# Optimization experiments

Hardware: AMD Instinct MI355X
Metric: run time of the kernel (lower is better)

## Reference

```python
import jax, jax.numpy as jnp
import numpy as np

N = 20000      # nodes
E = 160000     # edges
IN = 128       # in_channels
H = 16         # heads
C = 32         # hidden_channels (per-head dim)
HC = H * C     # 512
ED = 93        # edge_dim
B = 64         # graphs in batch


def setup_inputs() -> dict:
    key = jax.random.key(0)
    ks = jax.random.split(key, 32)
    w = lambda i, shape: jax.random.normal(ks[i], shape, dtype=jnp.float32) * 0.05
    inp = {
        "x": jax.random.normal(ks[0], (N, IN), dtype=jnp.float32),
        "edge_attr": jax.random.normal(ks[1], (E, ED), dtype=jnp.float32),
        "edge_index": jax.random.randint(ks[2], (2, E), 0, N),
        # sorted batch assignment; every graph id 0..B-1 is present
        "batch": (jnp.arange(N) * B) // N,
        # transformer1: in=IN
        "t1_Wq": w(3, (IN, HC)), "t1_bq": jnp.zeros((HC,), jnp.float32),
        "t1_Wk": w(4, (IN, HC)), "t1_bk": jnp.zeros((HC,), jnp.float32),
        "t1_Wv": w(5, (IN, HC)), "t1_bv": jnp.zeros((HC,), jnp.float32),
        "t1_We": w(6, (ED, HC)),
        "t1_Ws": w(7, (IN, HC)), "t1_bs": jnp.zeros((HC,), jnp.float32),
        # transformer2: in=HC
        "t2_Wq": w(8, (HC, HC)), "t2_bq": jnp.zeros((HC,), jnp.float32),
        "t2_Wk": w(9, (HC, HC)), "t2_bk": jnp.zeros((HC,), jnp.float32),
        "t2_Wv": w(10, (HC, HC)), "t2_bv": jnp.zeros((HC,), jnp.float32),
        "t2_We": w(11, (ED, HC)),
        "t2_Ws": w(12, (HC, HC)), "t2_bs": jnp.zeros((HC,), jnp.float32),
        # MLP head: fc1 (hidden*32 -> hidden*8), fc2 (hidden*8 -> hidden)
        "fc1_W": w(13, (2 * HC, 8 * C)), "fc1_b": jnp.zeros((8 * C,), jnp.float32),
        "fc2_W": w(14, (8 * C, C)), "fc2_b": jnp.zeros((C,), jnp.float32),
    }
    return inp


def _tconv(x, src, dst, edge_attr, Wq, bq, Wk, bk, Wv, bv, We, Ws, bs):
    # PyG TransformerConv, concat=True, beta=False, root_weight=True
    n = x.shape[0]
    q = (x @ Wq + bq).reshape(n, H, C)
    k = (x @ Wk + bk).reshape(n, H, C)
    v = (x @ Wv + bv).reshape(n, H, C)
    e = (edge_attr @ We).reshape(-1, H, C)          # lin_edge has no bias
    kj = k[src] + e                                  # [E,H,C]
    alpha = jnp.einsum('ehc,ehc->eh', q[dst], kj) / jnp.sqrt(jnp.float32(C))
    # segment softmax over incoming edges of each destination node
    amax = jax.ops.segment_max(alpha, dst, num_segments=n)
    ex = jnp.exp(alpha - amax[dst])
    denom = jax.ops.segment_sum(ex, dst, num_segments=n)
    a = ex / denom[dst]                              # [E,H]
    msg = (v[src] + e) * a[:, :, None]               # [E,H,C]
    agg = jax.ops.segment_sum(msg.reshape(-1, HC), dst, num_segments=n)
    return agg + x @ Ws + bs                         # root/skip connection


def _pool(x, batch):
    counts = jax.ops.segment_sum(jnp.ones((x.shape[0],), x.dtype), batch, num_segments=B)
    mean = jax.ops.segment_sum(x, batch, num_segments=B) / jnp.maximum(counts, 1.0)[:, None]
    mx = jax.ops.segment_max(x, batch, num_segments=B)
    return jnp.concatenate([mean, mx], axis=1)


def reference(x, edge_attr, edge_index, batch,
              t1_Wq, t1_bq, t1_Wk, t1_bk, t1_Wv, t1_bv, t1_We, t1_Ws, t1_bs,
              t2_Wq, t2_bq, t2_Wk, t2_bk, t2_Wv, t2_bv, t2_We, t2_Ws, t2_bs,
              fc1_W, fc1_b, fc2_W, fc2_b):
    src, dst = edge_index[0], edge_index[1]
    x1 = jax.nn.leaky_relu(_tconv(x, src, dst, edge_attr,
                                  t1_Wq, t1_bq, t1_Wk, t1_bk, t1_Wv, t1_bv,
                                  t1_We, t1_Ws, t1_bs), negative_slope=0.2)
    x3 = _pool(x1, batch)
    x2 = jax.nn.leaky_relu(_tconv(x1, src, dst, edge_attr,
                                  t2_Wq, t2_bq, t2_Wk, t2_bk, t2_Wv, t2_bv,
                                  t2_We, t2_Ws, t2_bs), negative_slope=0.2)
    x4 = _pool(x2, batch)
    h = x3 + x4                                      # [B, 2*HC]
    h = jax.nn.relu(h @ fc1_W + fc1_b)               # dropout = identity (eval)
    out = h @ fc2_W + fc2_b                          # [B, C]
    return out
```

## Files before the change

### kernel.cpp

```cpp
#include <hip/hip_runtime.h>
#include <cstdint>
#include <cstddef>

#define N_NODES 20000
#define N_EDGES 160000
#define IN_CH   128
#define NH      16
#define CD      32
#define HC      512
#define ED      93
#define EDP     96
#define NB      64
#define NCAT    2048
#define NSLICE  8
#define DEGSLK  2048

typedef __attribute__((ext_vector_type(8))) short short8;
typedef __attribute__((ext_vector_type(4))) float f32x4;
typedef unsigned short ushort_t;


__device__ inline ushort_t f2bf(float f) {
    unsigned int u = __float_as_uint(f);
    u = (u + 0x7FFF + ((u >> 16) & 1)) >> 16;
    return (ushort_t)u;
}
__device__ inline float bf2f(ushort_t u) {
    return __uint_as_float((unsigned)u << 16);
}
__device__ inline void unpack8(uint4 u, float* o) {
    o[0] = bf2f((ushort_t)(u.x & 0xffff)); o[1] = bf2f((ushort_t)(u.x >> 16));
    o[2] = bf2f((ushort_t)(u.y & 0xffff)); o[3] = bf2f((ushort_t)(u.y >> 16));
    o[4] = bf2f((ushort_t)(u.z & 0xffff)); o[5] = bf2f((ushort_t)(u.z >> 16));
    o[6] = bf2f((ushort_t)(u.w & 0xffff)); o[7] = bf2f((ushort_t)(u.w >> 16));
}
__device__ inline uint4 packf8(const float* f) {
    uint4 u;
    u.x = (unsigned)f2bf(f[0]) | ((unsigned)f2bf(f[1]) << 16);
    u.y = (unsigned)f2bf(f[2]) | ((unsigned)f2bf(f[3]) << 16);
    u.z = (unsigned)f2bf(f[4]) | ((unsigned)f2bf(f[5]) << 16);
    u.w = (unsigned)f2bf(f[6]) | ((unsigned)f2bf(f[7]) << 16);
    return u;
}

__device__ inline void gload_lds16(const void* g, void* l) {
    __builtin_amdgcn_global_load_lds(
        (const __attribute__((address_space(1))) void*)g,
        (__attribute__((address_space(3))) void*)l, 16, 0, 0);
}

__global__ void k_zero_i(int* __restrict__ p, int n) {
    int i = blockIdx.x * blockDim.x + threadIdx.x;
    int stride = gridDim.x * blockDim.x;
    for (; i < n; i += stride) p[i] = 0;
}

__global__ void k_cvt_x(const float* __restrict__ in, ushort_t* __restrict__ out, int n8) {
    int i = blockIdx.x * blockDim.x + threadIdx.x;
    int stride = gridDim.x * blockDim.x;
    for (; i < n8; i += stride) {
        const float4* p = (const float4*)(in + (size_t)i * 8);
        float4 a = p[0], b = p[1];
        float f[8] = {a.x, a.y, a.z, a.w, b.x, b.y, b.z, b.w};
        *(uint4*)(out + (size_t)i * 8) = packf8(f);
    }
}

__global__ void k_cvt_ea(const float* __restrict__ in, const int* __restrict__ perm,
                         ushort_t* __restrict__ out) {
    int i = blockIdx.x * blockDim.x + threadIdx.x;
    int stride = gridDim.x * blockDim.x;
    int total = N_EDGES * EDP;
    for (; i < total; i += stride) {
        int p = i / EDP, k = i - p * EDP;
        int e = perm[p];
        out[i] = (k < ED) ? f2bf(in[(size_t)e * ED + k]) : (ushort_t)0;
    }
}

__global__ __launch_bounds__(256) void k_cvt_wtT(
    const float* __restrict__ W0, const float* __restrict__ W1,
    const float* __restrict__ W2, const float* __restrict__ W3,
    ushort_t* __restrict__ Wt, int K, int N, int Kp) {
    __shared__ float tile[32][33];
    int z = blockIdx.z;
    const float* W = (z == 0) ? W0 : (z == 1) ? W1 : (z == 2) ? W2 : W3;
    ushort_t* out = Wt + (size_t)z * N * Kp;
    int n0 = blockIdx.x << 5;
    int k0 = blockIdx.y << 5;
    int r = threadIdx.x >> 5;
    int c = threadIdx.x & 31;
#pragma unroll
    for (int rr = 0; rr < 4; ++rr) {
        int k = k0 + r + rr * 8;
        tile[r + rr * 8][c] = (k < K) ? W[(size_t)k * N + n0 + c] : 0.f;
    }
    __syncthreads();
#pragma unroll
    for (int rr = 0; rr < 4; ++rr) {
        int n = n0 + r + rr * 8;
        out[(size_t)n * Kp + k0 + c] = f2bf(tile[c][r + rr * 8]);
    }
}

__global__ void k_bcat2(
    const float* __restrict__ b0q, const float* __restrict__ b0k,
    const float* __restrict__ b0v, const float* __restrict__ b0s,
    const float* __restrict__ b1q, const float* __restrict__ b1k,
    const float* __restrict__ b1v, const float* __restrict__ b1s,
    float* __restrict__ out) {
    int i = blockIdx.x * blockDim.x + threadIdx.x;
    if (i >= 2 * NCAT) return;
    int l = i >> 11, j = i & (NCAT - 1);
    int s = j >> 9, jj = j & 511;
    const float* b = (l == 0)
        ? ((s == 0) ? b0q : (s == 1) ? b0k : (s == 2) ? b0v : b0s)
        : ((s == 0) ? b1q : (s == 1) ? b1k : (s == 2) ? b1v : b1s);
    out[i] = b[jj];
}


__global__ void k_hist(const int* __restrict__ dst, int* __restrict__ deg) {
    int i = blockIdx.x * blockDim.x + threadIdx.x;
    if (i < N_EDGES) atomicAdd(&deg[dst[i]], 1);
}

__global__ __launch_bounds__(1024) void k_scan(const int* __restrict__ deg,
                                               int* __restrict__ rowptr,
                                               int* __restrict__ cursor) {
    __shared__ int part[1024];
    int t = threadIdx.x;
    int base = t * 20;
    int loc[20];
    int s = 0;
#pragma unroll
    for (int i = 0; i < 20; ++i) {
        int idx = base + i;
        int v = (idx < N_NODES) ? deg[idx] : 0;
        loc[i] = s; s += v;
    }
    part[t] = s;
    __syncthreads();
    for (int off = 1; off < 1024; off <<= 1) {
        int v = (t >= off) ? part[t - off] : 0;
        __syncthreads();
        part[t] += v;
        __syncthreads();
    }
    int pre = (t > 0) ? part[t - 1] : 0;
#pragma unroll
    for (int i = 0; i < 20; ++i) {
        int idx = base + i;
        if (idx < N_NODES) {
            int v = pre + loc[i];
            rowptr[idx] = v;
            cursor[idx] = v;
        }
    }
    if (t == 1023) rowptr[N_NODES] = part[1023];
}

__global__ void k_scatter(const int* __restrict__ src, const int* __restrict__ dst,
                          int* __restrict__ cursor, int* __restrict__ perm,
                          int* __restrict__ psrc) {
    int i = blockIdx.x * blockDim.x + threadIdx.x;
    if (i >= N_EDGES) return;
    int d = dst[i];
    int p = atomicAdd(&cursor[d], 1);
    perm[p] = i;
    psrc[p] = src[i];
}


__global__ __launch_bounds__(256) void k_mfma_gemm(
    const ushort_t* __restrict__ A, const ushort_t* __restrict__ Bt,
    const float* __restrict__ bias, ushort_t* __restrict__ Yb,
    int M, int K, int N) {
    __shared__ char smem[32768];
    char* As = smem;
    char* Bs = smem + 16384;

    int tid  = threadIdx.x;
    int lane = tid & 63, wave = tid >> 6;
    int l15 = lane & 15, lg = lane >> 4;
    int nt = N >> 7;
    int nwg = gridDim.x;
    int bid = blockIdx.x;
    int wg;
    if ((nwg & 7) == 0) { int cpx = nwg >> 3; wg = (bid & 7) * cpx + (bid >> 3); }
    else wg = bid;
    int bm = (wg / nt) * 128, bn = (wg % nt) * 128;
    int wm = (wave >> 1) * 64, wn = (wave & 1) * 64;

    f32x4 acc[4][4] = {};

    int sr = lane >> 3;
    int su = lane & 7;
    int gu = su ^ sr;

    for (int k0 = 0; k0 < K; k0 += 64) {
#pragma unroll
        for (int i = 0; i < 4; ++i) {
            int rloc = wave * 32 + i * 8;
            int row = rloc + sr;
            if (bm + row < M)
                gload_lds16(A + (size_t)(bm + row) * K + k0 + gu * 8, As + rloc * 128);
            gload_lds16(Bt + (size_t)(bn + row) * K + k0 + gu * 8, Bs + rloc * 128);
        }
        __syncthreads();

#pragma unroll
        for (int ks = 0; ks < 2; ++ks) {
            short8 af[4], bfr[4];
#pragma unroll
            for (int mr = 0; mr < 4; ++mr) {
                int r = wm + mr * 16 + l15;
                af[mr] = *(const short8*)(As + r * 128 + (((ks * 4 + lg) ^ (r & 7)) << 4));
            }
#pragma unroll
            for (int nc = 0; nc < 4; ++nc) {
                int r = wn + nc * 16 + l15;
                bfr[nc] = *(const short8*)(Bs + r * 128 + (((ks * 4 + lg) ^ (r & 7)) << 4));
            }
#pragma unroll
            for (int mr = 0; mr < 4; ++mr)
#pragma unroll
                for (int nc = 0; nc < 4; ++nc)
                    acc[mr][nc] = __builtin_amdgcn_mfma_f32_16x16x32_bf16(
                        af[mr], bfr[nc], acc[mr][nc], 0, 0, 0);
        }
        __syncthreads();
    }

    char* Cs = smem;
#pragma unroll
    for (int mr = 0; mr < 4; ++mr) {
#pragma unroll
        for (int nc = 0; nc < 4; ++nc) {
            int coll = wn + nc * 16 + l15;
            float b = bias ? bias[bn + coll] : 0.f;
            int u0 = coll >> 3;
#pragma unroll
            for (int j = 0; j < 4; ++j) {
                int row = wm + mr * 16 + lg * 4 + j;
                int u = u0 ^ (row & 7);
                *(ushort_t*)(Cs + row * 256 + (u << 4) + ((coll & 7) << 1)) =
                    f2bf(acc[mr][nc][j] + b);
            }
        }
    }
    __syncthreads();
    {
        int rsub = tid >> 4;
        int un   = tid & 15;
#pragma unroll
        for (int i = 0; i < 8; ++i) {
            int row = i * 16 + rsub;
            int gr = bm + row;
            if (gr < M) {
                int u = un ^ (row & 7);
                *(uint4*)(Yb + (size_t)gr * N + bn + un * 8) =
                    *(const uint4*)(Cs + row * 256 + (u << 4));
            }
        }
    }
}


__global__ __launch_bounds__(256) void k_egemm(
    const ushort_t* __restrict__ Ab, const ushort_t* __restrict__ Bt,
    ushort_t* __restrict__ Yb, int pbase, int ec) {
    __shared__ char smem[49152];
    char* As = smem;
    char* Bs = smem + 24576;

    int tid  = threadIdx.x;
    int lane = tid & 63, wave = tid >> 6;
    int l15 = lane & 15, lg = lane >> 4;
    int nwg = gridDim.x;
    int bid = blockIdx.x;
    int wg;
    if ((nwg & 7) == 0) { int cpx = nwg >> 3; wg = (bid & 7) * cpx + (bid >> 3); }
    else wg = bid;
    int bm = (wg >> 2) * 128;
    int n0 = (wg & 3) * 128;
    int wm = (wave >> 1) * 64, wn = (wave & 1) * 64;

    int srow = tid >> 1;
    int h    = tid & 1;
    int ssw  = ((srow >> 1) & 3) << 4;
    {
        int gm = bm + srow;
        uint4 va[6];
#pragma unroll
        for (int i = 0; i < 6; ++i) { va[i].x = va[i].y = va[i].z = va[i].w = 0; }
        if (gm < ec) {
            const uint4* ga = (const uint4*)(Ab + (size_t)(pbase + gm) * EDP + h * 48);
#pragma unroll
            for (int i = 0; i < 6; ++i) va[i] = ga[i];
        }
        char* dsta = As + srow * 192;
#pragma unroll
        for (int i = 0; i < 6; ++i) {
            int c = h * 96 + i * 16;
            *(uint4*)(dsta + ((c & ~63) | ((c & 63) ^ ssw))) = va[i];
        }
        uint4 vb[6];
        {
            const uint4* gb = (const uint4*)(Bt + (size_t)(n0 + srow) * EDP + h * 48);
#pragma unroll
            for (int i = 0; i < 6; ++i) vb[i] = gb[i];
        }
        char* dstb = Bs + srow * 192;
#pragma unroll
        for (int i = 0; i < 6; ++i) {
            int c = h * 96 + i * 16;
            *(uint4*)(dstb + ((c & ~63) | ((c & 63) ^ ssw))) = vb[i];
        }
    }
    __syncthreads();

    int fsw = ((l15 >> 1) & 3) << 4;

    f32x4 acc[4][4] = {};
#pragma unroll
    for (int ks = 0; ks < 3; ++ks) {
        short8 af[4], bfr[4];
#pragma unroll
        for (int mr = 0; mr < 4; ++mr) {
            int r = wm + mr * 16 + l15;
            int c = ks * 64 + ((lg * 16) ^ fsw);
            af[mr] = *(const short8*)(As + r * 192 + c);
        }
#pragma unroll
        for (int nc = 0; nc < 4; ++nc) {
            int r = wn + nc * 16 + l15;
            int c = ks * 64 + ((lg * 16) ^ fsw);
            bfr[nc] = *(const short8*)(Bs + r * 192 + c);
        }
#pragma unroll
        for (int mr = 0; mr < 4; ++mr)
#pragma unroll
            for (int nc = 0; nc < 4; ++nc)
                acc[mr][nc] = __builtin_amdgcn_mfma_f32_16x16x32_bf16(
                    af[mr], bfr[nc], acc[mr][nc], 0, 0, 0);
    }
    __syncthreads();

    char* Cs = smem;
#pragma unroll
    for (int mr = 0; mr < 4; ++mr) {
#pragma unroll
        for (int nc = 0; nc < 4; ++nc) {
            int col = wn + nc * 16 + l15;
#pragma unroll
            for (int j = 0; j < 4; ++j) {
                int row = wm + mr * 16 + lg * 4 + j;
                *(ushort_t*)(Cs + row * 288 + col * 2) = f2bf(acc[mr][nc][j]);
            }
        }
    }
    __syncthreads();

    {
        int rsub = tid >> 4;
        int un   = tid & 15;
#pragma unroll
        for (int i = 0; i < 8; ++i) {
            int row = i * 16 + rsub;
            if (bm + row < ec) {
                *(uint4*)(Yb + (size_t)(bm + row) * HC + n0 + un * 8) =
                    *(const uint4*)(Cs + row * 288 + un * 16);
            }
        }
    }
}


__global__ __launch_bounds__(128) void k_edge_fc(
    const ushort_t* __restrict__ qkvs, const ushort_t* __restrict__ eb,
    const int* __restrict__ psrc, const int* __restrict__ rowptr,
    ushort_t* __restrict__ xoutb, int e0, int elim) {
    int n = blockIdx.x;
    int beg = rowptr[n], end = rowptr[n + 1];
    if (beg < e0 || beg >= elim) return;

    int t = threadIdx.x;
    int w = t >> 6;
    int lane = t & 63;
    int c0 = lane * 8;
    int h = lane >> 2;

    float q[8];
    unpack8(*(const uint4*)(qkvs + (size_t)n * NCAT + c0), q);

    float mm = -1e30f, dd = 0.f, a[8];
#pragma unroll
    for (int j = 0; j < 8; ++j) a[j] = 0.f;

    int i = beg + w;
    uint4 ku4, vu4, eu4;
    if (i < end) {
        int sn = psrc[i];
        ku4 = *(const uint4*)(qkvs + (size_t)sn * NCAT + 512 + c0);
        vu4 = *(const uint4*)(qkvs + (size_t)sn * NCAT + 1024 + c0);
        eu4 = *(const uint4*)(eb + (size_t)(i - e0) * HC + c0);
    }
    while (i < end) {
        uint4 kc = ku4, vc = vu4, ec = eu4;
        int inext = i + 2;
        if (inext < end) {
            int sn2 = psrc[inext];
            ku4 = *(const uint4*)(qkvs + (size_t)sn2 * NCAT + 512 + c0);
            vu4 = *(const uint4*)(qkvs + (size_t)sn2 * NCAT + 1024 + c0);
            eu4 = *(const uint4*)(eb + (size_t)(inext - e0) * HC + c0);
        }
        float kk[8], vv[8], ee[8];
        unpack8(kc, kk); unpack8(vc, vv); unpack8(ec, ee);
        float part = 0.f;
#pragma unroll
        for (int j = 0; j < 8; ++j) part += q[j] * (kk[j] + ee[j]);
        part += __shfl_xor(part, 1);
        part += __shfl_xor(part, 2);
        float s = part * 0.17677669529663687f;
        float mn = fmaxf(mm, s);
        float sc = __expf(mm - mn);
        float p  = __expf(s - mn);
        dd = dd * sc + p;
        mm = mn;
#pragma unroll
        for (int j = 0; j < 8; ++j) a[j] = a[j] * sc + p * (vv[j] + ee[j]);
        i = inext;
    }

    __shared__ float sm_acc[512];
    __shared__ float sm_m[16];
    __shared__ float sm_d[16];
    if (w == 1) {
#pragma unroll
        for (int j = 0; j < 8; ++j) sm_acc[c0 + j] = a[j];
        if ((lane & 3) == 0) { sm_m[h] = mm; sm_d[h] = dd; }
    }
    __syncthreads();
    if (w == 0) {
        float m1 = sm_m[h], d1 = sm_d[h];
        float M = fmaxf(mm, m1);
        float sc0 = __expf(mm - M);
        float sc1 = __expf(m1 - M);
        dd = dd * sc0 + d1 * sc1;
        float inv = (dd > 0.f) ? 1.f / dd : 0.f;
        float sk[8];
        unpack8(*(const uint4*)(qkvs + (size_t)n * NCAT + 1536 + c0), sk);
        float o[8];
#pragma unroll
        for (int j = 0; j < 8; ++j) {
            float msg = (a[j] * sc0 + sm_acc[c0 + j] * sc1) * inv;
            float v = msg + sk[j];
            o[j] = v >= 0.f ? v : 0.2f * v;
        }
        *(uint4*)(xoutb + (size_t)n * HC + c0) = packf8(o);
    }
}


__global__ __launch_bounds__(256) void k_pool2(
    const ushort_t* __restrict__ xb, const int* __restrict__ batch,
    float* __restrict__ psum_p, float* __restrict__ pmax_p, int* __restrict__ cnt) {
    int b = blockIdx.x;
    int s = blockIdx.y;
    int lo = 0, hi = N_NODES;
    while (lo < hi) { int mid = (lo + hi) >> 1; if (batch[mid] < b) lo = mid + 1; else hi = mid; }
    int beg = lo;
    hi = N_NODES;
    while (lo < hi) { int mid = (lo + hi) >> 1; if (batch[mid] < b + 1) lo = mid + 1; else hi = mid; }
    int end = lo;
    if (s == 0 && threadIdx.x == 0) cnt[b] = end - beg;
    int cn = end - beg;
    int per = (cn + NSLICE - 1) / NSLICE;
    int nb = beg + s * per;
    int ne = nb + per; if (ne > end) ne = end;
    int c0 = threadIdx.x * 2;
    float s0 = 0.f, s1 = 0.f, m0 = -1e30f, m1 = -1e30f;
    for (int n = nb; n < ne; ++n) {
        unsigned int v = *(const unsigned int*)(xb + (size_t)n * HC + c0);
        float v0 = bf2f((ushort_t)(v & 0xffff));
        float v1 = bf2f((ushort_t)(v >> 16));
        s0 += v0; s1 += v1;
        m0 = fmaxf(m0, v0); m1 = fmaxf(m1, v1);
    }
    size_t o = ((size_t)s * NB + b) * HC + c0;
    psum_p[o] = s0; psum_p[o + 1] = s1;
    pmax_p[o] = m0; pmax_p[o + 1] = m1;
}

__global__ void k_poolfin(const float* __restrict__ psum_p, const float* __restrict__ pmax_p,
                          const int* __restrict__ cnt, float* __restrict__ hsum, int mode) {
    int i = blockIdx.x * blockDim.x + threadIdx.x;
    if (i >= NB * 1024) return;
    int b = i >> 10, c = i & 1023;
    float val;
    if (c < HC) {
        float s = 0.f;
#pragma unroll
        for (int sl = 0; sl < NSLICE; ++sl)
            s += psum_p[((size_t)sl * NB + b) * HC + c];
        int ct = cnt[b];
        val = s / (float)(ct > 0 ? ct : 1);
    } else {
        int cc = c - HC;
        float m = -1e30f;
#pragma unroll
        for (int sl = 0; sl < NSLICE; ++sl)
            m = fmaxf(m, pmax_p[((size_t)sl * NB + b) * HC + cc]);
        val = m;
    }
    if (mode == 0) hsum[i] = val;
    else hsum[i] += val;
}


__global__ __launch_bounds__(256) void k_head(
    const float* __restrict__ hsum, const float* __restrict__ fc1W,
    const float* __restrict__ fc1b, const float* __restrict__ fc2W,
    const float* __restrict__ fc2b, float* __restrict__ out) {
    int b = blockIdx.x;
    int j = threadIdx.x;
    __shared__ float hs[256];
    float acc = fc1b[j];
    const float* hin = hsum + (size_t)b * 1024;
    for (int k = 0; k < 1024; ++k) {
        acc += hin[k] * fc1W[(size_t)k * 256 + j];
    }
    hs[j] = fmaxf(acc, 0.f);
    __syncthreads();
    if (j < 32) {
        float o = fc2b[j];
        for (int k = 0; k < 256; ++k) o += hs[k] * fc2W[(size_t)k * 32 + j];
        out[b * 32 + j] = o;
    }
}


extern "C" void kernel_launch(void* const* d_in, const int* in_sizes, int n_in,
                              void* d_out, int out_size, void* d_ws, size_t ws_size,
                              hipStream_t stream) {
    const float* x      = (const float*)d_in[0];
    const float* ea     = (const float*)d_in[1];
    const int*   ei     = (const int*)d_in[2];
    const int*   batch  = (const int*)d_in[3];
    const int* src = ei;
    const int* dst = ei + N_EDGES;

    const float* t1_Wq = (const float*)d_in[4];
    const float* t1_bq = (const float*)d_in[5];
    const float* t1_Wk = (const float*)d_in[6];
    const float* t1_bk = (const float*)d_in[7];
    const float* t1_Wv = (const float*)d_in[8];
    const float* t1_bv = (const float*)d_in[9];
    const float* t1_We = (const float*)d_in[10];
    const float* t1_Ws = (const float*)d_in[11];
    const float* t1_bs = (const float*)d_in[12];
    const float* t2_Wq = (const float*)d_in[13];
    const float* t2_bq = (const float*)d_in[14];
    const float* t2_Wk = (const float*)d_in[15];
    const float* t2_bk = (const float*)d_in[16];
    const float* t2_Wv = (const float*)d_in[17];
    const float* t2_bv = (const float*)d_in[18];
    const float* t2_We = (const float*)d_in[19];
    const float* t2_Ws = (const float*)d_in[20];
    const float* t2_bs = (const float*)d_in[21];
    const float* fc1_W = (const float*)d_in[22];
    const float* fc1_b = (const float*)d_in[23];
    const float* fc2_W = (const float*)d_in[24];
    const float* fc2_b = (const float*)d_in[25];

    char* ws = (char*)d_ws;
    size_t off = 0;
    auto alloc = [&](size_t bytes) -> void* {
        void* p = ws + off;
        off = (off + bytes + 255) & ~(size_t)255;
        return p;
    };

    ushort_t* qkvs = (ushort_t*)alloc((size_t)N_NODES * NCAT * 2);
    float* psum_p = (float*)alloc((size_t)NSLICE * NB * HC * 4);
    float* pmax_p = (float*)alloc((size_t)NSLICE * NB * HC * 4);
    float* hsum = (float*)alloc((size_t)NB * 1024 * 4);
    int*   cnt  = (int*)alloc((size_t)NB * 4);
    int* deg    = (int*)alloc((size_t)N_NODES * 4);
    int* rowptr = (int*)alloc((size_t)(N_NODES + 1) * 4);
    int* cursor = (int*)alloc((size_t)N_NODES * 4);
    int* perm   = (int*)alloc((size_t)N_EDGES * 4);
    int* psrc   = (int*)alloc((size_t)N_EDGES * 4);
    ushort_t* x_b  = (ushort_t*)alloc((size_t)N_NODES * IN_CH * 2);
    ushort_t* x1_b = (ushort_t*)alloc((size_t)N_NODES * HC * 2);
    ushort_t* ea_b = (ushort_t*)alloc((size_t)N_EDGES * EDP * 2);
    ushort_t* wcat1 = (ushort_t*)alloc((size_t)NCAT * IN_CH * 2);
    ushort_t* wcat2 = (ushort_t*)alloc((size_t)NCAT * HC * 2);
    ushort_t* w_e   = (ushort_t*)alloc((size_t)2 * HC * EDP * 2);
    float* bcat = (float*)alloc((size_t)2 * NCAT * 4);

    size_t remain = (ws_size > off) ? (ws_size - off) : 0;
    ushort_t* eb = (ushort_t*)(ws + off);
    size_t per_edge = (size_t)HC * 2;
    long cap_rows = (long)(remain / per_edge);
    long S_max = cap_rows - DEGSLK;
    if (S_max < 1024) S_max = 1024;
    int nch = (int)((N_EDGES + S_max - 1) / S_max);
    if (nch < 1) nch = 1;
    int S = (N_EDGES + nch - 1) / nch;
    (void)in_sizes; (void)n_in; (void)out_size;

    hipLaunchKernelGGL(k_zero_i, dim3(79), dim3(256), 0, stream, deg, N_NODES);
    hipLaunchKernelGGL(k_hist, dim3((N_EDGES + 255) / 256), dim3(256), 0, stream, dst, deg);
    hipLaunchKernelGGL(k_scan, dim3(1), dim3(1024), 0, stream, deg, rowptr, cursor);
    hipLaunchKernelGGL(k_scatter, dim3((N_EDGES + 255) / 256), dim3(256), 0, stream,
                       src, dst, cursor, perm, psrc);

    hipLaunchKernelGGL(k_cvt_x, dim3(512), dim3(256), 0, stream, x, x_b,
                       N_NODES * IN_CH / 8);
    hipLaunchKernelGGL(k_cvt_ea, dim3(4096), dim3(256), 0, stream, ea, perm, ea_b);
    hipLaunchKernelGGL(k_cvt_wtT, dim3(HC / 32, IN_CH / 32, 4), dim3(256), 0, stream,
                       t1_Wq, t1_Wk, t1_Wv, t1_Ws, wcat1, IN_CH, HC, IN_CH);
    hipLaunchKernelGGL(k_cvt_wtT, dim3(HC / 32, HC / 32, 4), dim3(256), 0, stream,
                       t2_Wq, t2_Wk, t2_Wv, t2_Ws, wcat2, HC, HC, HC);
    hipLaunchKernelGGL(k_cvt_wtT, dim3(HC / 32, EDP / 32, 2), dim3(256), 0, stream,
                       t1_We, t2_We, t1_We, t1_We, w_e, ED, HC, EDP);
    hipLaunchKernelGGL(k_bcat2, dim3(16), dim3(256), 0, stream,
                       t1_bq, t1_bk, t1_bv, t1_bs, t2_bq, t2_bk, t2_bv, t2_bs, bcat);

    auto run_layer = [&](const ushort_t* xin_b, int Kin, const ushort_t* wcat,
                         const float* bc, const ushort_t* we,
                         ushort_t* xoutb, int poolmode) {
        int mt = (N_NODES + 127) / 128;
        int nt = NCAT / 128;
        hipLaunchKernelGGL(k_mfma_gemm, dim3(mt * nt), dim3(256), 0, stream,
                           xin_b, wcat, bc, qkvs, N_NODES, Kin, NCAT);

        for (int ci = 0; ci < nch; ++ci) {
            int e0 = ci * S;
            if (e0 >= N_EDGES) break;
            long ecl = (long)S + DEGSLK;
            if (ecl > N_EDGES - e0) ecl = N_EDGES - e0;
            int ecnt = (int)ecl;
            int gm = (ecnt + 127) / 128;
            hipLaunchKernelGGL(k_egemm, dim3(gm * 4), dim3(256), 0, stream,
                               ea_b, we, eb, e0, ecnt);
            int elim = (ci == nch - 1) ? (N_EDGES + 1) : (e0 + S);
            hipLaunchKernelGGL(k_edge_fc, dim3(N_NODES), dim3(128), 0, stream,
                               qkvs, eb, psrc, rowptr, xoutb, e0, elim);
        }

        hipLaunchKernelGGL(k_pool2, dim3(NB, NSLICE), dim3(256), 0, stream,
                           xoutb, batch, psum_p, pmax_p, cnt);
        hipLaunchKernelGGL(k_poolfin, dim3((NB * 1024 + 255) / 256), dim3(256), 0, stream,
                           psum_p, pmax_p, cnt, hsum, poolmode);
    };

    run_layer(x_b, IN_CH, wcat1, bcat, w_e, x1_b, 0);
    run_layer(x1_b, HC, wcat2, bcat + NCAT, w_e + (size_t)HC * EDP, x1_b, 1);

    hipLaunchKernelGGL(k_head, dim3(NB), dim3(256), 0, stream,
                       hsum, fc1_W, fc1_b, fc2_W, fc2_b, (float*)d_out);
}
```

Measured before the change: 559.9 us.

## Merge node QKVS GEMM and first edge-chunk GEMM into one launch

Adds a combined kernel that runs the node projection GEMM blocks and the first chunk's edge-attribute GEMM blocks in a single grid, dispatching on block index. This removes one kernel launch and lets the two independent GEMMs fill the GPU together rather than in sequence. The combined kernel uses 48KB of shared memory for all blocks, which may lower occupancy for the node GEMM part.

Result: faster. 545.6 us (-2.6%).

```diff
diff --git a/kernel.cpp b/kernel.cpp
--- a/kernel.cpp
+++ b/kernel.cpp
@@ -169,6 +169,202 @@
     int p = atomicAdd(&cursor[d], 1);
     perm[p] = i;
     psrc[p] = src[i];
+}
+
+
+__global__ __launch_bounds__(256) void k_mega(
+    const ushort_t* __restrict__ A, const ushort_t* __restrict__ Bt,
+    const float* __restrict__ bias, ushort_t* __restrict__ Yb,
+    int M, int K, int N, int nq,
+    const ushort_t* __restrict__ Ab, const ushort_t* __restrict__ Bte,
+    ushort_t* __restrict__ Ybe, int ec, int neg) {
+    __shared__ char smem[49152];
+    int tid  = threadIdx.x;
+    int lane = tid & 63, wave = tid >> 6;
+    int l15 = lane & 15, lg = lane >> 4;
+    int wm = (wave >> 1) * 64, wn = (wave & 1) * 64;
+
+    if (blockIdx.x < nq) {
+        char* As = smem;
+        char* Bs = smem + 16384;
+        int nt = N >> 7;
+        int bid = blockIdx.x;
+        int wg;
+        if ((nq & 7) == 0) { int cpx = nq >> 3; wg = (bid & 7) * cpx + (bid >> 3); }
+        else wg = bid;
+        int bm = (wg / nt) * 128, bn = (wg % nt) * 128;
+
+        f32x4 acc[4][4] = {};
+
+        int sr = lane >> 3;
+        int su = lane & 7;
+        int gu = su ^ sr;
+
+        for (int k0 = 0; k0 < K; k0 += 64) {
+#pragma unroll
+            for (int i = 0; i < 4; ++i) {
+                int rloc = wave * 32 + i * 8;
+                int row = rloc + sr;
+                if (bm + row < M)
+                    gload_lds16(A + (size_t)(bm + row) * K + k0 + gu * 8, As + rloc * 128);
+                gload_lds16(Bt + (size_t)(bn + row) * K + k0 + gu * 8, Bs + rloc * 128);
+            }
+            __syncthreads();
+
+#pragma unroll
+            for (int ks = 0; ks < 2; ++ks) {
+                short8 af[4], bfr[4];
+#pragma unroll
+                for (int mr = 0; mr < 4; ++mr) {
+                    int r = wm + mr * 16 + l15;
+                    af[mr] = *(const short8*)(As + r * 128 + (((ks * 4 + lg) ^ (r & 7)) << 4));
+                }
+#pragma unroll
+                for (int nc = 0; nc < 4; ++nc) {
+                    int r = wn + nc * 16 + l15;
+                    bfr[nc] = *(const short8*)(Bs + r * 128 + (((ks * 4 + lg) ^ (r & 7)) << 4));
+                }
+#pragma unroll
+                for (int mr = 0; mr < 4; ++mr)
+#pragma unroll
+                    for (int nc = 0; nc < 4; ++nc)
+                        acc[mr][nc] = __builtin_amdgcn_mfma_f32_16x16x32_bf16(
+                            af[mr], bfr[nc], acc[mr][nc], 0, 0, 0);
+            }
+            __syncthreads();
+        }
+
+        char* Cs = smem;
+#pragma unroll
+        for (int mr = 0; mr < 4; ++mr) {
+#pragma unroll
+            for (int nc = 0; nc < 4; ++nc) {
+                int coll = wn + nc * 16 + l15;
+                float b = bias ? bias[bn + coll] : 0.f;
+                int u0 = coll >> 3;
+#pragma unroll
+                for (int j = 0; j < 4; ++j) {
+                    int row = wm + mr * 16 + lg * 4 + j;
+                    int u = u0 ^ (row & 7);
+                    *(ushort_t*)(Cs + row * 256 + (u << 4) + ((coll & 7) << 1)) =
+                        f2bf(acc[mr][nc][j] + b);
+                }
+            }
+        }
+        __syncthreads();
+        {
+            int rsub = tid >> 4;
+            int un   = tid & 15;
+#pragma unroll
+            for (int i = 0; i < 8; ++i) {
+                int row = i * 16 + rsub;
+                int gr = bm + row;
+                if (gr < M) {
+                    int u = un ^ (row & 7);
+                    *(uint4*)(Yb + (size_t)gr * N + bn + un * 8) =
+                        *(const uint4*)(Cs + row * 256 + (u << 4));
+                }
+            }
+        }
+    } else {
+        char* As = smem;
+        char* Bs = smem + 24576;
+        int bid = blockIdx.x - nq;
+        int wg;
+        if ((neg & 7) == 0) { int cpx = neg >> 3; wg = (bid & 7) * cpx + (bid >> 3); }
+        else wg = bid;
+        int bm = (wg >> 2) * 128;
+        int n0 = (wg & 3) * 128;
+
+        int srow = tid >> 1;
+        int h    = tid & 1;
+        int ssw  = ((srow >> 1) & 3) << 4;
+        {
+            int gm = bm + srow;
+            uint4 va[6];
+#pragma unroll
+            for (int i = 0; i < 6; ++i) { va[i].x = va[i].y = va[i].z = va[i].w = 0; }
+            if (gm < ec) {
+                const uint4* ga = (const uint4*)(Ab + (size_t)gm * EDP + h * 48);
+#pragma unroll
+                for (int i = 0; i < 6; ++i) va[i] = ga[i];
+            }
+            char* dsta = As + srow * 192;
+#pragma unroll
+            for (int i = 0; i < 6; ++i) {
+                int c = h * 96 + i * 16;
+                *(uint4*)(dsta + ((c & ~63) | ((c & 63) ^ ssw))) = va[i];
+            }
+            uint4 vb[6];
+            {
+                const uint4* gb = (const uint4*)(Bte + (size_t)(n0 + srow) * EDP + h * 48);
+#pragma unroll
+                for (int i = 0; i < 6; ++i) vb[i] = gb[i];
+            }
+            char* dstb = Bs + srow * 192;
+#pragma unroll
+            for (int i = 0; i < 6; ++i) {
+                int c = h * 96 + i * 16;
+                *(uint4*)(dstb + ((c & ~63) | ((c & 63) ^ ssw))) = vb[i];
+            }
+        }
+        __syncthreads();
+
+        int fsw = ((l15 >> 1) & 3) << 4;
+
+        f32x4 acc[4][4] = {};
+#pragma unroll
+        for (int ks = 0; ks < 3; ++ks) {
+            short8 af[4], bfr[4];
+#pragma unroll
+            for (int mr = 0; mr < 4; ++mr) {
+                int r = wm + mr * 16 + l15;
+                int c = ks * 64 + ((lg * 16) ^ fsw);
+                af[mr] = *(const short8*)(As + r * 192 + c);
+            }
+#pragma unroll
+            for (int nc = 0; nc < 4; ++nc) {
+                int r = wn + nc * 16 + l15;
+                int c = ks * 64 + ((lg * 16) ^ fsw);
+                bfr[nc] = *(const short8*)(Bs + r * 192 + c);
+            }
+#pragma unroll
+            for (int mr = 0; mr < 4; ++mr)
+#pragma unroll
+                for (int nc = 0; nc < 4; ++nc)
+                    acc[mr][nc] = __builtin_amdgcn_mfma_f32_16x16x32_bf16(
+                        af[mr], bfr[nc], acc[mr][nc], 0, 0, 0);
+        }
+        __syncthreads();
+
+        char* Cs = smem;
+#pragma unroll
+        for (int mr = 0; mr < 4; ++mr) {
+#pragma unroll
+            for (int nc = 0; nc < 4; ++nc) {
+                int col = wn + nc * 16 + l15;
+#pragma unroll
+                for (int j = 0; j < 4; ++j) {
+                    int row = wm + mr * 16 + lg * 4 + j;
+                    *(ushort_t*)(Cs + row * 288 + col * 2) = f2bf(acc[mr][nc][j]);
+                }
+            }
+        }
+        __syncthreads();
+
+        {
+            int rsub = tid >> 4;
+            int un   = tid & 15;
+#pragma unroll
+            for (int i = 0; i < 8; ++i) {
+                int row = i * 16 + rsub;
+                if (bm + row < ec) {
+                    *(uint4*)(Ybe + (size_t)(bm + row) * HC + n0 + un * 8) =
+                        *(const uint4*)(Cs + row * 288 + un * 16);
+                }
+            }
+        }
+    }
 }
 
 
@@ -634,10 +830,21 @@
                          ushort_t* xoutb, int poolmode) {
         int mt = (N_NODES + 127) / 128;
         int nt = NCAT / 128;
-        hipLaunchKernelGGL(k_mfma_gemm, dim3(mt * nt), dim3(256), 0, stream,
-                           xin_b, wcat, bc, qkvs, N_NODES, Kin, NCAT);
-
-        for (int ci = 0; ci < nch; ++ci) {
+        int nq = mt * nt;
+
+        long ecl0 = (long)S + DEGSLK;
+        if (ecl0 > N_EDGES) ecl0 = N_EDGES;
+        int ecnt0 = (int)ecl0;
+        int neg0 = ((ecnt0 + 127) / 128) * 4;
+        hipLaunchKernelGGL(k_mega, dim3(nq + neg0), dim3(256), 0, stream,
+                           xin_b, wcat, bc, qkvs, N_NODES, Kin, NCAT, nq,
+                           ea_b, we, eb, ecnt0, neg0);
+        {
+            int elim0 = (nch == 1) ? (N_EDGES + 1) : S;
+            hipLaunchKernelGGL(k_edge_fc, dim3(N_NODES), dim3(128), 0, stream,
+                               qkvs, eb, psrc, rowptr, xoutb, 0, elim0);
+        }
+        for (int ci = 1; ci < nch; ++ci) {
             int e0 = ci * S;
             if (e0 >= N_EDGES) break;
             long ecl = (long)S + DEGSLK;
```

## Merge node QKVS GEMM and first edge-projection GEMM into one launch

Applied to the files above, without the earlier changes.

Adds a combined kernel whose first blocks compute the node QKVS projection and whose remaining blocks compute the edge-feature projection for the first edge chunk, so both GEMMs share one launch and fill the GPU together. The edge GEMM now reuses the generic async-LDS GEMM path, with the edge weight padded to a K of 128 and the A rows read at stride 96. Reading 128 columns from 96-wide rows pulls in the next row's data, which is cancelled by the zero weight padding. A small zeroed tail is added after the edge-attribute buffer so the last row's over-read stays in bounds. The cost is a third more MFMA work on the edge GEMM from the padding.

After: 577.4 us. 3.1% more time.

```diff
diff --git a/kernel.cpp b/kernel.cpp
--- a/kernel.cpp
+++ b/kernel.cpp
@@ -10,6 +10,7 @@
 #define HC      512
 #define ED      93
 #define EDP     96
+#define KEP     128
 #define NB      64
 #define NCAT    2048
 #define NSLICE  8
@@ -172,10 +173,118 @@
 }
 
 
-__global__ __launch_bounds__(256) void k_mfma_gemm(
+__global__ __launch_bounds__(256) void k_mega(
     const ushort_t* __restrict__ A, const ushort_t* __restrict__ Bt,
     const float* __restrict__ bias, ushort_t* __restrict__ Yb,
-    int M, int K, int N) {
+    int M, int K, int N, int nq,
+    const ushort_t* __restrict__ Ab, const ushort_t* __restrict__ Bte,
+    ushort_t* __restrict__ Ybe, int ec, int neg) {
+    __shared__ char smem[32768];
+    char* As = smem;
+    char* Bs = smem + 16384;
+
+    int tid  = threadIdx.x;
+    int lane = tid & 63, wave = tid >> 6;
+    int l15 = lane & 15, lg = lane >> 4;
+    int wm = (wave >> 1) * 64, wn = (wave & 1) * 64;
+
+    const ushort_t* Ap; const ushort_t* Bp; const float* bp; ushort_t* Yp;
+    int Mv, Kl, Nv, lda, ldb, bid, nwg;
+    if ((int)blockIdx.x < nq) {
+        Ap = A; Bp = Bt; bp = bias; Yp = Yb;
+        Mv = M; Kl = K; Nv = N; lda = K; ldb = K;
+        bid = blockIdx.x; nwg = nq;
+    } else {
+        Ap = Ab; Bp = Bte; bp = nullptr; Yp = Ybe;
+        Mv = ec; Kl = KEP; Nv = HC; lda = EDP; ldb = KEP;
+        bid = blockIdx.x - nq; nwg = neg;
+    }
+    int wg;
+    if ((nwg & 7) == 0) { int cpx = nwg >> 3; wg = (bid & 7) * cpx + (bid >> 3); }
+    else wg = bid;
+    int nt = Nv >> 7;
+    int bm = (wg / nt) * 128, bn = (wg % nt) * 128;
+
+    f32x4 acc[4][4] = {};
+
+    int sr = lane >> 3;
+    int su = lane & 7;
+    int gu = su ^ sr;
+
+    for (int k0 = 0; k0 < Kl; k0 += 64) {
+#pragma unroll
+        for (int i = 0; i < 4; ++i) {
+            int rloc = wave * 32 + i * 8;
+            int row = rloc + sr;
+            if (bm + row < Mv)
+                gload_lds16(Ap + (size_t)(bm + row) * lda + k0 + gu * 8, As + rloc * 128);
+            gload_lds16(Bp + (size_t)(bn + row) * ldb + k0 + gu * 8, Bs + rloc * 128);
+        }
+        __syncthreads();
+
+#pragma unroll
+        for (int ks = 0; ks < 2; ++ks) {
+            short8 af[4], bfr[4];
+#pragma unroll
+            for (int mr = 0; mr < 4; ++mr) {
+                int r = wm + mr * 16 + l15;
+                af[mr] = *(const short8*)(As + r * 128 + (((ks * 4 + lg) ^ (r & 7)) << 4));
+            }
+#pragma unroll
+            for (int nc = 0; nc < 4; ++nc) {
+                int r = wn + nc * 16 + l15;
+                bfr[nc] = *(const short8*)(Bs + r * 128 + (((ks * 4 + lg) ^ (r & 7)) << 4));
+            }
+#pragma unroll
+            for (int mr = 0; mr < 4; ++mr)
+#pragma unroll
+                for (int nc = 0; nc < 4; ++nc)
+                    acc[mr][nc] = __builtin_amdgcn_mfma_f32_16x16x32_bf16(
+                        af[mr], bfr[nc], acc[mr][nc], 0, 0, 0);
+        }
+        __syncthreads();
+    }
+
+    char* Cs = smem;
+#pragma unroll
+    for (int mr = 0; mr < 4; ++mr) {
+#pragma unroll
+        for (int nc = 0; nc < 4; ++nc) {
+            int coll = wn + nc * 16 + l15;
+            float b = bp ? bp[bn + coll] : 0.f;
+            int u0 = coll >> 3;
+#pragma unroll
+            for (int j = 0; j < 4; ++j) {
+                int row = wm + mr * 16 + lg * 4 + j;
+                int u = u0 ^ (row & 7);
+                *(ushort_t*)(Cs + row * 256 + (u << 4) + ((coll & 7) << 1)) =
+                    f2bf(acc[mr][nc][j] + b);
+            }
+        }
+    }
+    __syncthreads();
+    {
+        int rsub = tid >> 4;
+        int un   = tid & 15;
+#pragma unroll
+        for (int i = 0; i < 8; ++i) {
+            int row = i * 16 + rsub;
+            int gr = bm + row;
+            if (gr < Mv) {
+                int u = un ^ (row & 7);
+                *(uint4*)(Yp + (size_t)gr * Nv + bn + un * 8) =
+                    *(const uint4*)(Cs + row * 256 + (u << 4));
+            }
+        }
+    }
+}
+
+
+__global__ __launch_bounds__(256) void k_mfma_gemm(
+    const ushort_t* __restrict__ A, int lda,
+    const ushort_t* __restrict__ Bt, int ldb,
+    const float* __restrict__ bias, ushort_t* __restrict__ Yb,
+    int M, int Kl, int N) {
     __shared__ char smem[32768];
     char* As = smem;
     char* Bs = smem + 16384;
@@ -198,14 +307,14 @@
     int su = lane & 7;
     int gu = su ^ sr;
 
-    for (int k0 = 0; k0 < K; k0 += 64) {
+    for (int k0 = 0; k0 < Kl; k0 += 64) {
 #pragma unroll
         for (int i = 0; i < 4; ++i) {
             int rloc = wave * 32 + i * 8;
             int row = rloc + sr;
             if (bm + row < M)
-                gload_lds16(A + (size_t)(bm + row) * K + k0 + gu * 8, As + rloc * 128);
-            gload_lds16(Bt + (size_t)(bn + row) * K + k0 + gu * 8, Bs + rloc * 128);
+                gload_lds16(A + (size_t)(bm + row) * lda + k0 + gu * 8, As + rloc * 128);
+            gload_lds16(Bt + (size_t)(bn + row) * ldb + k0 + gu * 8, Bs + rloc * 128);
         }
         __syncthreads();
 
@@ -261,116 +370,6 @@
                 int u = un ^ (row & 7);
                 *(uint4*)(Yb + (size_t)gr * N + bn + un * 8) =
                     *(const uint4*)(Cs + row * 256 + (u << 4));
-            }
-        }
-    }
-}
-
-
-__global__ __launch_bounds__(256) void k_egemm(
-    const ushort_t* __restrict__ Ab, const ushort_t* __restrict__ Bt,
-    ushort_t* __restrict__ Yb, int pbase, int ec) {
-    __shared__ char smem[49152];
-    char* As = smem;
-    char* Bs = smem + 24576;
-
-    int tid  = threadIdx.x;
-    int lane = tid & 63, wave = tid >> 6;
-    int l15 = lane & 15, lg = lane >> 4;
-    int nwg = gridDim.x;
-    int bid = blockIdx.x;
-    int wg;
-    if ((nwg & 7) == 0) { int cpx = nwg >> 3; wg = (bid & 7) * cpx + (bid >> 3); }
-    else wg = bid;
-    int bm = (wg >> 2) * 128;
-    int n0 = (wg & 3) * 128;
-    int wm = (wave >> 1) * 64, wn = (wave & 1) * 64;
-
-    int srow = tid >> 1;
-    int h    = tid & 1;
-    int ssw  = ((srow >> 1) & 3) << 4;
-    {
-        int gm = bm + srow;
-        uint4 va[6];
-#pragma unroll
-        for (int i = 0; i < 6; ++i) { va[i].x = va[i].y = va[i].z = va[i].w = 0; }
-        if (gm < ec) {
-            const uint4* ga = (const uint4*)(Ab + (size_t)(pbase + gm) * EDP + h * 48);
-#pragma unroll
-            for (int i = 0; i < 6; ++i) va[i] = ga[i];
-        }
-        char* dsta = As + srow * 192;
-#pragma unroll
-        for (int i = 0; i < 6; ++i) {
-            int c = h * 96 + i * 16;
-            *(uint4*)(dsta + ((c & ~63) | ((c & 63) ^ ssw))) = va[i];
-        }
-        uint4 vb[6];
-        {
-            const uint4* gb = (const uint4*)(Bt + (size_t)(n0 + srow) * EDP + h * 48);
-#pragma unroll
-            for (int i = 0; i < 6; ++i) vb[i] = gb[i];
-        }
-        char* dstb = Bs + srow * 192;
-#pragma unroll
-        for (int i = 0; i < 6; ++i) {
-            int c = h * 96 + i * 16;
-            *(uint4*)(dstb + ((c & ~63) | ((c & 63) ^ ssw))) = vb[i];
-        }
-    }
-    __syncthreads();
-
-    int fsw = ((l15 >> 1) & 3) << 4;
-
-    f32x4 acc[4][4] = {};
-#pragma unroll
-    for (int ks = 0; ks < 3; ++ks) {
-        short8 af[4], bfr[4];
-#pragma unroll
-        for (int mr = 0; mr < 4; ++mr) {
-            int r = wm + mr * 16 + l15;
-            int c = ks * 64 + ((lg * 16) ^ fsw);
-            af[mr] = *(const short8*)(As + r * 192 + c);
-        }
-#pragma unroll
-        for (int nc = 0; nc < 4; ++nc) {
-            int r = wn + nc * 16 + l15;
-            int c = ks * 64 + ((lg * 16) ^ fsw);
-            bfr[nc] = *(const short8*)(Bs + r * 192 + c);
-        }
-#pragma unroll
-        for (int mr = 0; mr < 4; ++mr)
-#pragma unroll
-            for (int nc = 0; nc < 4; ++nc)
-                acc[mr][nc] = __builtin_amdgcn_mfma_f32_16x16x32_bf16(
-                    af[mr], bfr[nc], acc[mr][nc], 0, 0, 0);
-    }
-    __syncthreads();
-
-    char* Cs = smem;
-#pragma unroll
-    for (int mr = 0; mr < 4; ++mr) {
-#pragma unroll
-        for (int nc = 0; nc < 4; ++nc) {
-            int col = wn + nc * 16 + l15;
-#pragma unroll
-            for (int j = 0; j < 4; ++j) {
-                int row = wm + mr * 16 + lg * 4 + j;
-                *(ushort_t*)(Cs + row * 288 + col * 2) = f2bf(acc[mr][nc][j]);
-            }
-        }
-    }
-    __syncthreads();
-
-    {
-        int rsub = tid >> 4;
-        int un   = tid & 15;
-#pragma unroll
-        for (int i = 0; i < 8; ++i) {
-            int row = i * 16 + rsub;
-            if (bm + row < ec) {
-                *(uint4*)(Yb + (size_t)(bm + row) * HC + n0 + un * 8) =
-                    *(const uint4*)(Cs + row * 288 + un * 16);
             }
         }
     }
@@ -594,10 +593,10 @@
     int* psrc   = (int*)alloc((size_t)N_EDGES * 4);
     ushort_t* x_b  = (ushort_t*)alloc((size_t)N_NODES * IN_CH * 2);
     ushort_t* x1_b = (ushort_t*)alloc((size_t)N_NODES * HC * 2);
-    ushort_t* ea_b = (ushort_t*)alloc((size_t)N_EDGES * EDP * 2);
+    ushort_t* ea_b = (ushort_t*)alloc((size_t)N_EDGES * EDP * 2 + 256);
     ushort_t* wcat1 = (ushort_t*)alloc((size_t)NCAT * IN_CH * 2);
     ushort_t* wcat2 = (ushort_t*)alloc((size_t)NCAT * HC * 2);
-    ushort_t* w_e   = (ushort_t*)alloc((size_t)2 * HC * EDP * 2);
+    ushort_t* w_e   = (ushort_t*)alloc((size_t)2 * HC * KEP * 2);
     float* bcat = (float*)alloc((size_t)2 * NCAT * 4);
 
     size_t remain = (ws_size > off) ? (ws_size - off) : 0;
@@ -620,12 +619,14 @@
     hipLaunchKernelGGL(k_cvt_x, dim3(512), dim3(256), 0, stream, x, x_b,
                        N_NODES * IN_CH / 8);
     hipLaunchKernelGGL(k_cvt_ea, dim3(4096), dim3(256), 0, stream, ea, perm, ea_b);
+    hipLaunchKernelGGL(k_zero_i, dim3(1), dim3(64), 0, stream,
+                       (int*)(ea_b + (size_t)N_EDGES * EDP), 64);
     hipLaunchKernelGGL(k_cvt_wtT, dim3(HC / 32, IN_CH / 32, 4), dim3(256), 0, stream,
                        t1_Wq, t1_Wk, t1_Wv, t1_Ws, wcat1, IN_CH, HC, IN_CH);
     hipLaunchKernelGGL(k_cvt_wtT, dim3(HC / 32, HC / 32, 4), dim3(256), 0, stream,
                        t2_Wq, t2_Wk, t2_Wv, t2_Ws, wcat2, HC, HC, HC);
-    hipLaunchKernelGGL(k_cvt_wtT, dim3(HC / 32, EDP / 32, 2), dim3(256), 0, stream,
-                       t1_We, t2_We, t1_We, t1_We, w_e, ED, HC, EDP);
+    hipLaunchKernelGGL(k_cvt_wtT, dim3(HC / 32, KEP / 32, 2), dim3(256), 0, stream,
+                       t1_We, t2_We, t1_We, t1_We, w_e, ED, HC, KEP);
     hipLaunchKernelGGL(k_bcat2, dim3(16), dim3(256), 0, stream,
                        t1_bq, t1_bk, t1_bv, t1_bs, t2_bq, t2_bk, t2_bv, t2_bs, bcat);
 
@@ -634,18 +635,30 @@
                          ushort_t* xoutb, int poolmode) {
         int mt = (N_NODES + 127) / 128;
         int nt = NCAT / 128;
-        hipLaunchKernelGGL(k_mfma_gemm, dim3(mt * nt), dim3(256), 0, stream,
-                           xin_b, wcat, bc, qkvs, N_NODES, Kin, NCAT);
-
-        for (int ci = 0; ci < nch; ++ci) {
+        int nq = mt * nt;
+
+        long ecl0 = (long)S + DEGSLK;
+        if (ecl0 > N_EDGES) ecl0 = N_EDGES;
+        int ecnt0 = (int)ecl0;
+        int neg0 = ((ecnt0 + 127) / 128) * 4;
+        hipLaunchKernelGGL(k_mega, dim3(nq + neg0), dim3(256), 0, stream,
+                           xin_b, wcat, bc, qkvs, N_NODES, Kin, NCAT, nq,
+                           ea_b, we, eb, ecnt0, neg0);
+        {
+            int elim0 = (nch == 1) ? (N_EDGES + 1) : S;
+            hipLaunchKernelGGL(k_edge_fc, dim3(N_NODES), dim3(128), 0, stream,
+                               qkvs, eb, psrc, rowptr, xoutb, 0, elim0);
+        }
+        for (int ci = 1; ci < nch; ++ci) {
             int e0 = ci * S;
             if (e0 >= N_EDGES) break;
             long ecl = (long)S + DEGSLK;
             if (ecl > N_EDGES - e0) ecl = N_EDGES - e0;
             int ecnt = (int)ecl;
             int gm = (ecnt + 127) / 128;
-            hipLaunchKernelGGL(k_egemm, dim3(gm * 4), dim3(256), 0, stream,
-                               ea_b, we, eb, e0, ecnt);
+            hipLaunchKernelGGL(k_mfma_gemm, dim3(gm * 4), dim3(256), 0, stream,
+                               ea_b + (size_t)e0 * EDP, EDP, we, KEP,
+                               (const float*)nullptr, eb, ecnt, KEP, HC);
             int elim = (ci == nch - 1) ? (N_EDGES + 1) : (e0 + S);
             hipLaunchKernelGGL(k_edge_fc, dim3(N_NODES), dim3(128), 0, stream,
                                qkvs, eb, psrc, rowptr, xoutb, e0, elim);
@@ -658,7 +671,7 @@
     };
 
     run_layer(x_b, IN_CH, wcat1, bcat, w_e, x1_b, 0);
-    run_layer(x1_b, HC, wcat2, bcat + NCAT, w_e + (size_t)HC * EDP, x1_b, 1);
+    run_layer(x1_b, HC, wcat2, bcat + NCAT, w_e + (size_t)HC * KEP, x1_b, 1);
 
     hipLaunchKernelGGL(k_head, dim3(NB), dim3(256), 0, stream,
                        hsum, fc1_W, fc1_b, fc2_W, fc2_b, (float*)d_out);
```
